# Performance work log

Hardware: AMD Instinct MI355X
Metric: run time of the kernel (lower is better)

The kernel has to match this reference:

```python
import jax, jax.numpy as jnp
import numpy as np

N_NODES = 50000
N_EDGES = 1600000
D = 64
L = 4
ALPHA = 0.1


def setup_inputs() -> dict:
    key = jax.random.key(0)
    ks = jax.random.split(key, 6)
    x = jax.random.normal(ks[0], (N_NODES, D), dtype=jnp.float32)
    w = jax.random.uniform(ks[1], (N_EDGES,), dtype=jnp.float32)
    # linear layer params, scaled ~ 1/sqrt(fan_in)
    W = jax.random.normal(ks[2], (L, D, D), dtype=jnp.float32) * (1.0 / np.sqrt(D))
    b = jnp.zeros((L, D), dtype=jnp.float32)
    # GPR temp schedule: alpha*(1-alpha)^k, last = (1-alpha)^L
    temp = ALPHA * (1.0 - ALPHA) ** np.arange(L + 1)
    temp[-1] = (1.0 - ALPHA) ** L
    temp = jnp.asarray(temp, dtype=jnp.float32)
    src = jax.random.randint(ks[3], (N_EDGES,), 0, N_NODES, dtype=jnp.int32)
    dst = jax.random.randint(ks[4], (N_EDGES,), 0, N_NODES, dtype=jnp.int32)
    return {"x": x, "w": w, "W": W, "b": b, "temp": temp, "src": src, "dst": dst}


def reference(x, w, W, b, temp, src, dst):
    # Eval mode: dropout / dropout_adj are identity; edge_attn=False.
    n = x.shape[0]
    hidden = x * temp[0]
    num_layers = W.shape[0]
    for i in range(num_layers):
        # linear: h = x @ W_i^T + b_i
        h = jnp.einsum('nd,od->no', x, W[i]) + b[i]
        # u_mul_e + sum: gather src features, scale by edge weight, scatter-sum to dst
        m = h[src] * w[:, None]                       # [E, D]
        x = jax.ops.segment_sum(m, dst, num_segments=n)  # [N, D]
        x = jax.nn.relu(x)
        hidden = hidden + x * temp[i + 1]
    return hidden
```

## Files before the change

### kernel.cpp

```cpp
#include <hip/hip_runtime.h>
#include <hip/hip_fp16.h>

#define NN 50000
#define NE 1600000
#define DD 64
#define NBK 782
#define TILE 4096
#define NTB 391
#define SCAP 3072

typedef _Float16 half8 __attribute__((ext_vector_type(8)));
typedef float float4v __attribute__((ext_vector_type(4)));

__global__ __launch_bounds__(256) void wswz_kernel(const float* __restrict__ W,
                                                   _Float16* __restrict__ Wswz,
                                                   int* __restrict__ gcur) {
    int flat = blockIdx.x * 256 + threadIdx.x;
    if (blockIdx.x == 0) {
        for (int k = threadIdx.x; k < NBK; k += 256) gcur[k] = 0;
    }
    int l = flat >> 12, r = flat & 4095;
    int j = r & 7, lane = (r >> 3) & 63, kt = (r >> 9) & 1, nt = r >> 10;
    int n = nt * 16 + (lane & 15);
    int k = kt * 32 + ((lane >> 4) * 8) + j;
    Wswz[flat] = (_Float16)W[l * 4096 + n * 64 + k];
}

__global__ __launch_bounds__(256) void fill_kernel(const int* __restrict__ src,
                                                   const int* __restrict__ dst,
                                                   const float* __restrict__ w,
                                                   int* __restrict__ gcur,
                                                   unsigned int* __restrict__ tmp) {
    __shared__ unsigned int data[TILE];
    __shared__ unsigned short bktl[TILE];
    __shared__ int cnt[NBK], bas[NBK], rnk[NBK];
    __shared__ int sc[1024];
    int t = threadIdx.x;
    for (int k = t; k < NBK; k += 256) { cnt[k] = 0; rnk[k] = 0; }
    __syncthreads();
    int base = blockIdx.x * TILE;
    unsigned int er_e[TILE / 256];
    int er_b[TILE / 256];
#pragma unroll
    for (int k = 0; k < TILE / 256; ++k) {
        int i = base + k * 256 + t;
        if (i < NE) {
            int d = dst[i];
            unsigned int wq = (unsigned int)(w[i] * 1024.0f);
            if (wq > 1023u) wq = 1023u;
            er_e[k] = (unsigned int)src[i] | ((unsigned int)(d & 63) << 16) | (wq << 22);
            er_b[k] = d >> 6;
            atomicAdd(&cnt[er_b[k]], 1);
        }
    }
    __syncthreads();
    for (int k = t; k < NBK; k += 256) {
        int c = cnt[k];
        bas[k] = c ? atomicAdd(&gcur[k], c) : 0;
    }
    for (int k = t; k < 1024; k += 256) sc[k] = (k < NBK) ? cnt[k] : 0;
    __syncthreads();
    for (int s = 1; s < 1024; s <<= 1) {
        int v0[4];
#pragma unroll
        for (int j = 0; j < 4; ++j) {
            int idx = t + j * 256;
            v0[j] = (idx >= s) ? sc[idx - s] : 0;
        }
        __syncthreads();
#pragma unroll
        for (int j = 0; j < 4; ++j) sc[t + j * 256] += v0[j];
        __syncthreads();
    }
#pragma unroll
    for (int k = 0; k < TILE / 256; ++k) {
        int i = base + k * 256 + t;
        if (i < NE) {
            int b = er_b[k];
            int r = atomicAdd(&rnk[b], 1);
            int pos = (sc[b] - cnt[b]) + r;
            data[pos] = er_e[k];
            bktl[pos] = (unsigned short)b;
        }
    }
    __syncthreads();
    int tot = NE - base; if (tot > TILE) tot = TILE;
    for (int idx = t; idx < tot; idx += 256) {
        int b = bktl[idx];
        int lb = sc[b] - cnt[b];
        tmp[(size_t)b * SCAP + bas[b] + (idx - lb)] = data[idx];
    }
}

__global__ __launch_bounds__(256) void sort_kernel(const unsigned int* __restrict__ tmp,
                                                   const int* __restrict__ gcur,
                                                   unsigned int* __restrict__ csr,
                                                   int2* __restrict__ off2) {
    __shared__ int cnt[64], nb[64], pos[64];
    int b = blockIdx.x, t = threadIdx.x;
    int beg = b * SCAP, n = gcur[b];
    if (t < 64) cnt[t] = 0;
    __syncthreads();
    for (int i = t; i < n; i += 256) {
        unsigned int e = tmp[beg + i];
        atomicAdd(&cnt[(e >> 16) & 63u], 1);
    }
    __syncthreads();
    if (t == 0) {
        int a = 0;
        for (int k = 0; k < 64; ++k) { nb[k] = a; pos[k] = a; a += cnt[k]; }
    }
    __syncthreads();
    for (int i = t; i < n; i += 256) {
        unsigned int e = tmp[beg + i];
        int d = (int)((e >> 16) & 63u);
        float wf = ((float)(e >> 22) + 0.5f) * (1.0f / 1024.0f);
        unsigned int wh = (unsigned int)__half_as_ushort(__float2half_rn(wf));
        int r = atomicAdd(&pos[d], 1);
        csr[beg + r] = (e & 0xffffu) | (wh << 16);
    }
    __syncthreads();
    if (t < 64) {
        int node = b * 64 + t;
        if (node < NN) {
            int2 oe;
            oe.x = beg + nb[t];
            oe.y = beg + nb[t] + cnt[t];
            off2[node] = oe;
        }
    }
}

__global__ __launch_bounds__(256) void gemm0_mfma(const float* __restrict__ x32,
                                                  const _Float16* __restrict__ Wg,
                                                  const float* __restrict__ bl,
                                                  _Float16* __restrict__ h) {
    int t = threadIdx.x;
    int wave = t >> 6, lane = t & 63;
    int m = lane & 15, q = lane >> 4;
    int node0 = blockIdx.x * 64 + wave * 16;
    int arow = node0 + m; if (arow >= NN) arow = NN - 1;
    const float4* xr = (const float4*)(x32 + (size_t)arow * 64);
    float4 f0 = xr[2 * q], f1 = xr[2 * q + 1];
    float4 f2 = xr[8 + 2 * q], f3 = xr[8 + 2 * q + 1];
    half8 a0, a1;
    a0[0] = (_Float16)f0.x; a0[1] = (_Float16)f0.y; a0[2] = (_Float16)f0.z; a0[3] = (_Float16)f0.w;
    a0[4] = (_Float16)f1.x; a0[5] = (_Float16)f1.y; a0[6] = (_Float16)f1.z; a0[7] = (_Float16)f1.w;
    a1[0] = (_Float16)f2.x; a1[1] = (_Float16)f2.y; a1[2] = (_Float16)f2.z; a1[3] = (_Float16)f2.w;
    a1[4] = (_Float16)f3.x; a1[5] = (_Float16)f3.y; a1[6] = (_Float16)f3.z; a1[7] = (_Float16)f3.w;
    const half8* Wf = (const half8*)Wg;
    float4v acc[4];
#pragma unroll
    for (int nt = 0; nt < 4; ++nt) acc[nt] = (float4v){0.f, 0.f, 0.f, 0.f};
#pragma unroll
    for (int nt = 0; nt < 4; ++nt) {
        half8 b0 = Wf[(nt * 2 + 0) * 64 + lane];
        half8 b1 = Wf[(nt * 2 + 1) * 64 + lane];
        acc[nt] = __builtin_amdgcn_mfma_f32_16x16x32_f16(a0, b0, acc[nt], 0, 0, 0);
        acc[nt] = __builtin_amdgcn_mfma_f32_16x16x32_f16(a1, b1, acc[nt], 0, 0, 0);
    }
#pragma unroll
    for (int nt = 0; nt < 4; ++nt) {
        float bv = bl[nt * 16 + m];
#pragma unroll
        for (int r = 0; r < 4; ++r) {
            int node = node0 + q * 4 + r;
            if (node < NN)
                h[(size_t)node * 64 + nt * 16 + m] = (_Float16)(acc[nt][r] + bv);
        }
    }
}

__global__ __launch_bounds__(256) void pull_fused(const uint4* __restrict__ h16,
                                                  const unsigned int* __restrict__ csr,
                                                  const int2* __restrict__ off2,
                                                  float4* __restrict__ out,
                                                  const float4* __restrict__ x32,
                                                  const float* __restrict__ temp,
                                                  const _Float16* __restrict__ Wg,
                                                  const float* __restrict__ bl,
                                                  _Float16* __restrict__ hout,
                                                  int layer) {
    __shared__ _Float16 vsh[16 * 72];
    int t = threadIdx.x;
    int lane = t & 63;
    int slot = lane >> 4, g = (lane >> 3) & 1, sub = lane & 7;
    int node0 = blockIdx.x * 16;
    int nloc = (t >> 6) * 4 + slot;
    int node = node0 + nloc;
    bool tail = (node0 + 16 > NN);
    if (tail) {
        for (int k = t; k < 16 * 72; k += 256) vsh[k] = (_Float16)0.f;
        __syncthreads();
    }

    int nclamp = node < NN ? node : NN - 1;
    int2 oe = off2[nclamp];
    int deg = (node < NN) ? (oe.y - oe.x) : 0;
    int beg = oe.x;
    int dmax = deg;
    dmax = max(dmax, __shfl_xor(dmax, 16));
    dmax = max(dmax, __shfl_xor(dmax, 32));
    int sl = lane & 15;
    float acc[8];
#pragma unroll
    for (int k = 0; k < 8; ++k) acc[k] = 0.f;

    int chunks = (dmax + 15) >> 4;
    unsigned int e = (sl < deg) ? csr[beg + sl] : 0u;
    for (int c = 0; c < chunks; ++c) {
        int nidx = ((c + 1) << 4) + sl;
        unsigned int enext = (nidx < deg) ? csr[beg + nidx] : 0u;
#pragma unroll
        for (int j = 0; j < 8; ++j) {
            unsigned int ej = (unsigned int)__shfl((int)e, (slot << 4) + j * 2 + g);
            int s = (int)(ej & 0xffffu);
            __half wh = __ushort_as_half((unsigned short)(ej >> 16));
            uint4 hv = h16[(size_t)s * 8 + sub];
            const __half* hp = (const __half*)&hv;
            float wf = (float)wh;
#pragma unroll
            for (int k = 0; k < 8; ++k)
                acc[k] += (float)hp[k] * wf;
        }
        e = enext;
    }
#pragma unroll
    for (int k = 0; k < 8; ++k) acc[k] += __shfl_xor(acc[k], 8);

    if (g == 0 && node < NN) {
        float tk = temp[layer + 1];
        float v[8];
#pragma unroll
        for (int k = 0; k < 8; ++k) v[k] = fmaxf(acc[k], 0.f);
        __half2 p[4];
#pragma unroll
        for (int k = 0; k < 4; ++k) p[k] = __floats2half2_rn(v[2 * k], v[2 * k + 1]);
        *(uint4*)&vsh[nloc * 72 + sub * 8] = *(const uint4*)p;
        int gi = node * 16 + sub * 2;
        float4 o0, o1;
        if (layer == 0) {
            float t0 = temp[0];
            float4 a = x32[gi], bq = x32[gi + 1];
            o0.x = a.x * t0;  o0.y = a.y * t0;  o0.z = a.z * t0;  o0.w = a.w * t0;
            o1.x = bq.x * t0; o1.y = bq.y * t0; o1.z = bq.z * t0; o1.w = bq.w * t0;
        } else {
            o0 = out[gi]; o1 = out[gi + 1];
        }
        o0.x += v[0] * tk; o0.y += v[1] * tk; o0.z += v[2] * tk; o0.w += v[3] * tk;
        o1.x += v[4] * tk; o1.y += v[5] * tk; o1.z += v[6] * tk; o1.w += v[7] * tk;
        out[gi]     = o0;
        out[gi + 1] = o1;
    }

    if (Wg != nullptr) {
        __syncthreads();
        int wave = t >> 6;
        int m = lane & 15, q = lane >> 4;
        half8 a0 = *(const half8*)&vsh[m * 72 + q * 8];
        half8 a1 = *(const half8*)&vsh[m * 72 + 32 + q * 8];
        const half8* Wf = (const half8*)Wg;
        half8 b0 = Wf[(wave * 2 + 0) * 64 + lane];
        half8 b1 = Wf[(wave * 2 + 1) * 64 + lane];
        float4v d = (float4v){0.f, 0.f, 0.f, 0.f};
        d = __builtin_amdgcn_mfma_f32_16x16x32_f16(a0, b0, d, 0, 0, 0);
        d = __builtin_amdgcn_mfma_f32_16x16x32_f16(a1, b1, d, 0, 0, 0);
        float bv = bl[wave * 16 + m];
#pragma unroll
        for (int r = 0; r < 4; ++r) {
            int n2 = node0 + q * 4 + r;
            if (n2 < NN)
                hout[(size_t)n2 * 64 + wave * 16 + m] = (_Float16)(d[r] + bv);
        }
    }
}

extern "C" void kernel_launch(void* const* d_in, const int* in_sizes, int n_in,
                              void* d_out, int out_size, void* d_ws, size_t ws_size,
                              hipStream_t stream) {
    const float* x    = (const float*)d_in[0];
    const float* w    = (const float*)d_in[1];
    const float* W    = (const float*)d_in[2];
    const float* b    = (const float*)d_in[3];
    const float* temp = (const float*)d_in[4];
    const int*   src  = (const int*)d_in[5];
    const int*   dst  = (const int*)d_in[6];
    float* out = (float*)d_out;

    _Float16*     hA   = (_Float16*)d_ws;
    _Float16*     hB   = hA + (size_t)NN * DD;
    unsigned int* csr  = (unsigned int*)(hB + (size_t)NN * DD);
    unsigned int* tmp  = csr + (size_t)NBK * SCAP;
    int*          gcur = (int*)(tmp + (size_t)NBK * SCAP);
    int2*         off2 = (int2*)(gcur + NBK);
    _Float16*     Wswz = (_Float16*)(off2 + NN);

    wswz_kernel<<<64, 256, 0, stream>>>(W, Wswz, gcur);
    fill_kernel<<<NTB, 256, 0, stream>>>(src, dst, w, gcur, tmp);
    sort_kernel<<<NBK, 256, 0, stream>>>(tmp, gcur, csr, off2);

    gemm0_mfma<<<NBK, 256, 0, stream>>>(x, Wswz, b, hA);

    const int PG = (NN + 15) / 16;
    _Float16* hin  = hA;
    _Float16* hout = hB;
    for (int l = 0; l < 4; ++l) {
        const _Float16* Wn = (l < 3) ? (Wswz + (size_t)(l + 1) * 4096) : nullptr;
        const float*    bn = (l < 3) ? (b + (size_t)(l + 1) * DD) : nullptr;
        pull_fused<<<PG, 256, 0, stream>>>(
            (const uint4*)hin, csr, off2, (float4*)out, (const float4*)x,
            temp, Wn, bn, hout, l);
        _Float16* sw = hin; hin = hout; hout = sw;
    }
}
```

Measured before the change: 228.4 us.

## Fuse bucket sort with first GEMM and enlarge fill tiles

Merges the per-bucket counting sort and the layer-0 MFMA GEMM into one kernel, which drops a launch and lets the x loads be issued early so their latency overlaps the sort. The sort now caches its bucket slice in shared memory instead of reading tmp from global memory twice. The fill kernel doubles its tile to 8192 edges with half as many blocks, and it re-reads dst/src/w in a second pass instead of holding them in registers. The cost is extra global re-reads, fewer fill blocks, and more shared memory per sort block.

```diff
diff --git a/kernel.cpp b/kernel.cpp
--- a/kernel.cpp
+++ b/kernel.cpp
@@ -5,8 +5,8 @@
 #define NE 1600000
 #define DD 64
 #define NBK 782
-#define TILE 4096
-#define NTB 391
+#define TILE 8192
+#define NTB 196
 #define SCAP 3072
 
 typedef _Float16 half8 __attribute__((ext_vector_type(8)));
@@ -39,47 +39,42 @@
     for (int k = t; k < NBK; k += 256) { cnt[k] = 0; rnk[k] = 0; }
     __syncthreads();
     int base = blockIdx.x * TILE;
-    unsigned int er_e[TILE / 256];
-    int er_b[TILE / 256];
-#pragma unroll
+#pragma unroll 8
+    for (int k = 0; k < TILE / 256; ++k) {
+        int i = base + k * 256 + t;
+        if (i < NE) atomicAdd(&cnt[dst[i] >> 6], 1);
+    }
+    __syncthreads();
+    for (int k = t; k < NBK; k += 256) {
+        int c = cnt[k];
+        bas[k] = c ? atomicAdd(&gcur[k], c) : 0;
+    }
+    for (int k = t; k < 1024; k += 256) sc[k] = (k < NBK) ? cnt[k] : 0;
+    __syncthreads();
+    for (int s = 1; s < 1024; s <<= 1) {
+        int v0[4];
+#pragma unroll
+        for (int j = 0; j < 4; ++j) {
+            int idx = t + j * 256;
+            v0[j] = (idx >= s) ? sc[idx - s] : 0;
+        }
+        __syncthreads();
+#pragma unroll
+        for (int j = 0; j < 4; ++j) sc[t + j * 256] += v0[j];
+        __syncthreads();
+    }
+#pragma unroll 4
     for (int k = 0; k < TILE / 256; ++k) {
         int i = base + k * 256 + t;
         if (i < NE) {
             int d = dst[i];
+            int b = d >> 6;
             unsigned int wq = (unsigned int)(w[i] * 1024.0f);
             if (wq > 1023u) wq = 1023u;
-            er_e[k] = (unsigned int)src[i] | ((unsigned int)(d & 63) << 16) | (wq << 22);
-            er_b[k] = d >> 6;
-            atomicAdd(&cnt[er_b[k]], 1);
-        }
-    }
-    __syncthreads();
-    for (int k = t; k < NBK; k += 256) {
-        int c = cnt[k];
-        bas[k] = c ? atomicAdd(&gcur[k], c) : 0;
-    }
-    for (int k = t; k < 1024; k += 256) sc[k] = (k < NBK) ? cnt[k] : 0;
-    __syncthreads();
-    for (int s = 1; s < 1024; s <<= 1) {
-        int v0[4];
-#pragma unroll
-        for (int j = 0; j < 4; ++j) {
-            int idx = t + j * 256;
-            v0[j] = (idx >= s) ? sc[idx - s] : 0;
-        }
-        __syncthreads();
-#pragma unroll
-        for (int j = 0; j < 4; ++j) sc[t + j * 256] += v0[j];
-        __syncthreads();
-    }
-#pragma unroll
-    for (int k = 0; k < TILE / 256; ++k) {
-        int i = base + k * 256 + t;
-        if (i < NE) {
-            int b = er_b[k];
+            unsigned int e = (unsigned int)src[i] | ((unsigned int)(d & 63) << 16) | (wq << 22);
             int r = atomicAdd(&rnk[b], 1);
             int pos = (sc[b] - cnt[b]) + r;
-            data[pos] = er_e[k];
+            data[pos] = e;
             bktl[pos] = (unsigned short)b;
         }
     }
@@ -92,17 +87,32 @@
     }
 }
 
-__global__ __launch_bounds__(256) void sort_kernel(const unsigned int* __restrict__ tmp,
-                                                   const int* __restrict__ gcur,
-                                                   unsigned int* __restrict__ csr,
-                                                   int2* __restrict__ off2) {
+__global__ __launch_bounds__(256) void sortgemm_kernel(const unsigned int* __restrict__ tmp,
+                                                       const int* __restrict__ gcur,
+                                                       unsigned int* __restrict__ csr,
+                                                       int2* __restrict__ off2,
+                                                       const float* __restrict__ x32,
+                                                       const _Float16* __restrict__ Wg,
+                                                       const float* __restrict__ bl,
+                                                       _Float16* __restrict__ h) {
+    __shared__ unsigned int sdata[SCAP];
     __shared__ int cnt[64], nb[64], pos[64];
     int b = blockIdx.x, t = threadIdx.x;
+
+    int wave = t >> 6, lane = t & 63;
+    int m = lane & 15, q = lane >> 4;
+    int node0 = b * 64 + wave * 16;
+    int arow = node0 + m; if (arow >= NN) arow = NN - 1;
+    const float4* xr = (const float4*)(x32 + (size_t)arow * 64);
+    float4 f0 = xr[2 * q], f1 = xr[2 * q + 1];
+    float4 f2 = xr[8 + 2 * q], f3 = xr[8 + 2 * q + 1];
+
     int beg = b * SCAP, n = gcur[b];
     if (t < 64) cnt[t] = 0;
     __syncthreads();
     for (int i = t; i < n; i += 256) {
         unsigned int e = tmp[beg + i];
+        sdata[i] = e;
         atomicAdd(&cnt[(e >> 16) & 63u], 1);
     }
     __syncthreads();
@@ -112,14 +122,13 @@
     }
     __syncthreads();
     for (int i = t; i < n; i += 256) {
-        unsigned int e = tmp[beg + i];
+        unsigned int e = sdata[i];
         int d = (int)((e >> 16) & 63u);
         float wf = ((float)(e >> 22) + 0.5f) * (1.0f / 1024.0f);
         unsigned int wh = (unsigned int)__half_as_ushort(__float2half_rn(wf));
         int r = atomicAdd(&pos[d], 1);
         csr[beg + r] = (e & 0xffffu) | (wh << 16);
     }
-    __syncthreads();
     if (t < 64) {
         int node = b * 64 + t;
         if (node < NN) {
@@ -129,20 +138,7 @@
             off2[node] = oe;
         }
     }
-}
-
-__global__ __launch_bounds__(256) void gemm0_mfma(const float* __restrict__ x32,
-                                                  const _Float16* __restrict__ Wg,
-                                                  const float* __restrict__ bl,
-                                                  _Float16* __restrict__ h) {
-    int t = threadIdx.x;
-    int wave = t >> 6, lane = t & 63;
-    int m = lane & 15, q = lane >> 4;
-    int node0 = blockIdx.x * 64 + wave * 16;
-    int arow = node0 + m; if (arow >= NN) arow = NN - 1;
-    const float4* xr = (const float4*)(x32 + (size_t)arow * 64);
-    float4 f0 = xr[2 * q], f1 = xr[2 * q + 1];
-    float4 f2 = xr[8 + 2 * q], f3 = xr[8 + 2 * q + 1];
+
     half8 a0, a1;
     a0[0] = (_Float16)f0.x; a0[1] = (_Float16)f0.y; a0[2] = (_Float16)f0.z; a0[3] = (_Float16)f0.w;
     a0[4] = (_Float16)f1.x; a0[5] = (_Float16)f1.y; a0[6] = (_Float16)f1.z; a0[7] = (_Float16)f1.w;
@@ -297,9 +293,7 @@
 
     wswz_kernel<<<64, 256, 0, stream>>>(W, Wswz, gcur);
     fill_kernel<<<NTB, 256, 0, stream>>>(src, dst, w, gcur, tmp);
-    sort_kernel<<<NBK, 256, 0, stream>>>(tmp, gcur, csr, off2);
-
-    gemm0_mfma<<<NBK, 256, 0, stream>>>(x, Wswz, b, hA);
+    sortgemm_kernel<<<NBK, 256, 0, stream>>>(tmp, gcur, csr, off2, x, Wswz, b, hA);
 
     const int PG = (NN + 15) / 16;
     _Float16* hin  = hA;
```

Result: slower. 241.2 us (+5.6%).
